# Kernel tuning notes

Hardware: AMD Instinct MI355X
Metric: run time of the kernel (lower is better)

Reference implementation:

```python
import jax, jax.numpy as jnp
import numpy as np
from jax.ops import segment_sum, segment_max

N_NODES = 10000
N_EDGES = 160000
N_GRAPHS = 32
IN_DIM = 128
HID = 256
HEADS = 4


def setup_inputs() -> dict:
    key = jax.random.key(0)
    ks = jax.random.split(key, 12)
    x = jax.random.normal(ks[0], (N_NODES, IN_DIM), dtype=jnp.float32)
    edge_index = jax.random.randint(ks[1], (2, N_EDGES), 0, N_NODES, dtype=jnp.int64)
    batch = jnp.sort(jax.random.randint(ks[2], (N_NODES,), 0, N_GRAPHS, dtype=jnp.int64))
    s = 0.05
    params = {
        "W1": jax.random.normal(ks[3], (IN_DIM, HID), dtype=jnp.float32) * s,
        "b1": jnp.zeros((HID,), dtype=jnp.float32),
        "W2": jax.random.normal(ks[4], (HID, HID), dtype=jnp.float32) * s,
        "b2": jnp.zeros((HID,), dtype=jnp.float32),
        "Wg": jax.random.normal(ks[5], (HID, HEADS * HID), dtype=jnp.float32) * s,
        "att_src": jax.random.normal(ks[6], (HEADS, HID), dtype=jnp.float32) * s,
        "att_dst": jax.random.normal(ks[7], (HEADS, HID), dtype=jnp.float32) * s,
        "bg": jnp.zeros((HID,), dtype=jnp.float32),
        "W_heads": jax.random.normal(ks[8], (HID, 4), dtype=jnp.float32) * s,
        "b_heads": jnp.zeros((4,), dtype=jnp.float32),
    }
    return {"x": x, "edge_index": edge_index, "batch": batch, **params}


def _add_self_loops(edge_index, n):
    loop = jnp.arange(n, dtype=edge_index.dtype)
    src = jnp.concatenate([edge_index[0], loop])
    dst = jnp.concatenate([edge_index[1], loop])
    return src, dst


def _gcn_conv(x, W, b, src, dst, n):
    # PyG GCNConv: add self-loops, symmetric normalization D^-1/2 A D^-1/2
    h = x @ W                                   # [N, out]
    deg = segment_sum(jnp.ones_like(src, dtype=h.dtype), dst, num_segments=n)
    dinv = jax.lax.rsqrt(jnp.maximum(deg, 1e-12))
    coef = dinv[src] * dinv[dst]                # [E+N]
    out = segment_sum(h[src] * coef[:, None], dst, num_segments=n)
    return out + b


def _gat_conv(x, Wg, att_src, att_dst, bg, src, dst, n):
    # PyG GATConv(heads=4, concat=False): mean over heads, leaky_relu slope 0.2
    h = (x @ Wg).reshape(n, HEADS, HID)         # [N, H, C]
    a_src = jnp.einsum('nhc,hc->nh', h, att_src)
    a_dst = jnp.einsum('nhc,hc->nh', h, att_dst)
    e = jax.nn.leaky_relu(a_src[src] + a_dst[dst], 0.2)   # [E+N, H]
    m = segment_max(e, dst, num_segments=n)
    e = jnp.exp(e - m[dst])
    z = segment_sum(e, dst, num_segments=n)
    alpha = e / (z[dst] + 1e-16)                # softmax over edges into each dst
    out = segment_sum(h[src] * alpha[:, :, None], dst, num_segments=n)  # [N, H, C]
    return out.mean(axis=1) + bg


def reference(x, edge_index, batch, W1, b1, W2, b2, Wg, att_src, att_dst, bg, W_heads, b_heads):
    n = x.shape[0]
    src, dst = _add_self_loops(edge_index, n)
    h1 = jax.nn.relu(_gcn_conv(x, W1, b1, src, dst, n))
    h2 = jax.nn.relu(_gcn_conv(h1, W2, b2, src, dst, n))
    h3 = jax.nn.relu(_gat_conv(h2, Wg, att_src, att_dst, bg, src, dst, n))
    # global_mean_pool
    ones = jnp.ones((n,), dtype=h3.dtype)
    cnt = segment_sum(ones, batch, num_segments=N_GRAPHS)
    pooled = segment_sum(h3, batch, num_segments=N_GRAPHS) / jnp.maximum(cnt, 1.0)[:, None]
    # four scalar heads stacked: cols = [energy_absorption, elastic_modulus, ballistic_limit, penetration_resistance]
    return pooled @ W_heads + b_heads           # [G, 4]
```

## Files before the change

kernel.cpp:

```cpp
#include <hip/hip_runtime.h>
#include <cmath>

#define IN_DIM 128
#define HID 256
#define NHEADS 4
#define NGRAPHS 32

typedef unsigned short u16;
typedef __attribute__((ext_vector_type(8))) short bfrag8;
typedef __attribute__((ext_vector_type(4))) float f32x4;

__device__ __forceinline__ u16 f2bf(float x) {
  unsigned u = __float_as_uint(x);
  unsigned r = (u + 0x7fffu + ((u >> 16) & 1u)) >> 16;
  return (u16)r;
}
__device__ __forceinline__ float bf2f(u16 v) {
  return __uint_as_float(((unsigned)v) << 16);
}
__device__ __forceinline__ float lof(unsigned u) { return __uint_as_float(u << 16); }
__device__ __forceinline__ float hif(unsigned u) { return __uint_as_float(u & 0xffff0000u); }
__device__ __forceinline__ float lrelu02(float x) { return x > 0.f ? x : 0.2f * x; }

#define GACC(U, W)                                                   \
  acc[0] += (W) * lof((U).x); acc[1] += (W) * hif((U).x);            \
  acc[2] += (W) * lof((U).y); acc[3] += (W) * hif((U).y);            \
  acc[4] += (W) * lof((U).z); acc[5] += (W) * hif((U).z);            \
  acc[6] += (W) * lof((U).w); acc[7] += (W) * hif((U).w);

__global__ __launch_bounds__(256) void count_edges_k(const int* __restrict__ dst,
                                                     int* __restrict__ cnt, int E) {
  int i = blockIdx.x * 256 + threadIdx.x;
  if (i < E) atomicAdd(&cnt[dst[i]], 1);
}

__global__ __launch_bounds__(1024) void scan_k(const int* __restrict__ cnt,
                                               int* __restrict__ row_ptr,
                                               float* __restrict__ dinv, int n) {
  __shared__ int s_w[16];
  __shared__ int s_tot;
  int tid = threadIdx.x;
  int wv = tid >> 6, lane = tid & 63;
  int carry = 0;
  int nch = (n + 1023) >> 10;
  for (int c = 0; c < nch; c++) {
    int i = (c << 10) + tid;
    int v = (i < n) ? cnt[i] : 0;
    int incl = v;
    #pragma unroll
    for (int off = 1; off < 64; off <<= 1) {
      int t = __shfl_up(incl, off);
      if (lane >= off) incl += t;
    }
    if (lane == 63) s_w[wv] = incl;
    __syncthreads();
    if (tid < 16) {
      int sv = s_w[tid];
      int si = sv;
      #pragma unroll
      for (int off = 1; off < 16; off <<= 1) {
        int t = __shfl_up(si, off, 16);
        if (tid >= off) si += t;
      }
      s_w[tid] = si - sv;
      if (tid == 15) s_tot = si;
    }
    __syncthreads();
    int excl = incl - v + s_w[wv] + carry;
    if (i < n) {
      row_ptr[i] = excl;
      dinv[i] = rsqrtf((float)(v + 1));
    }
    carry += s_tot;
    __syncthreads();
  }
  if (tid == 0) row_ptr[n] = carry;
}

__global__ __launch_bounds__(256) void fill_csr_k(const int* __restrict__ src,
                                                  const int* __restrict__ dst,
                                                  const int* __restrict__ row_ptr,
                                                  int* __restrict__ cursor,
                                                  int* __restrict__ csr_src, int E) {
  int i = blockIdx.x * 256 + threadIdx.x;
  if (i < E) {
    int d = dst[i];
    int p = atomicAdd(&cursor[d], 1);
    csr_src[row_ptr[d] + p] = src[i];
  }
}

__device__ void pack_a_dev(const float* __restrict__ A, u16* __restrict__ Ap,
                           int K, int KT, int wid, int lane) {
  int fm = wid / KT, kt = wid - fm * KT;
  int m = fm * 16 + (lane & 15);
  int kb = kt * 32 + (lane >> 4) * 8;
  const float* src = A + (size_t)m * K + kb;
  float4 v0 = *(const float4*)src;
  float4 v1 = *(const float4*)(src + 4);
  float vv[8] = {v0.x, v0.y, v0.z, v0.w, v1.x, v1.y, v1.z, v1.w};
  u16 hi[8], lo[8];
  #pragma unroll
  for (int j = 0; j < 8; j++) {
    u16 h = f2bf(vv[j]);
    hi[j] = h;
    lo[j] = f2bf(vv[j] - bf2f(h));
  }
  u16* dstp = Ap + ((size_t)fm * KT + kt) * 1024 + lane * 8;
  *(ushort4*)(dstp)       = make_ushort4(hi[0], hi[1], hi[2], hi[3]);
  *(ushort4*)(dstp + 4)   = make_ushort4(hi[4], hi[5], hi[6], hi[7]);
  *(ushort4*)(dstp + 512) = make_ushort4(lo[0], lo[1], lo[2], lo[3]);
  *(ushort4*)(dstp + 516) = make_ushort4(lo[4], lo[5], lo[6], lo[7]);
}

__device__ void pack_b_dev(const float* __restrict__ B, u16* __restrict__ Bp,
                           int N, int KT, int wid, int lane) {
  int fn = wid / KT, kt = wid - fn * KT;
  int n = fn * 16 + (lane & 15);
  int kb = kt * 32 + (lane >> 4) * 8;
  float vv[8];
  #pragma unroll
  for (int j = 0; j < 8; j++) vv[j] = B[(size_t)(kb + j) * N + n];
  u16 hi[8], lo[8];
  #pragma unroll
  for (int j = 0; j < 8; j++) {
    u16 h = f2bf(vv[j]);
    hi[j] = h;
    lo[j] = f2bf(vv[j] - bf2f(h));
  }
  u16* dstp = Bp + ((size_t)fn * KT + kt) * 1024 + lane * 8;
  *(ushort4*)(dstp)       = make_ushort4(hi[0], hi[1], hi[2], hi[3]);
  *(ushort4*)(dstp + 4)   = make_ushort4(hi[4], hi[5], hi[6], hi[7]);
  *(ushort4*)(dstp + 512) = make_ushort4(lo[0], lo[1], lo[2], lo[3]);
  *(ushort4*)(dstp + 516) = make_ushort4(lo[4], lo[5], lo[6], lo[7]);
}

__global__ __launch_bounds__(256) void prep_k(const float* __restrict__ x,
                                              const float* __restrict__ W1,
                                              const float* __restrict__ W2,
                                              const float* __restrict__ Wg,
                                              const float* __restrict__ att_src,
                                              const float* __restrict__ att_dst,
                                              u16* __restrict__ xp,
                                              u16* __restrict__ w1p,
                                              u16* __restrict__ w2p,
                                              u16* __restrict__ wgp,
                                              float* __restrict__ w_s,
                                              float* __restrict__ w_d, int NFM) {
  __shared__ float red_s[4][NHEADS];
  __shared__ float red_d[4][NHEADS];
  int b = blockIdx.x;
  int tid = threadIdx.x;
  int lane = tid & 63;
  int XB = NFM;
  if (b < XB) {
    int wid = b * 4 + (tid >> 6);
    if (wid < NFM * 4) pack_a_dev(x, xp, IN_DIM, 4, wid, lane);
  } else if (b < XB + 16) {
    pack_b_dev(W1, w1p, HID, 4, (b - XB) * 4 + (tid >> 6), lane);
  } else if (b < XB + 48) {
    pack_b_dev(W2, w2p, HID, 8, (b - XB - 16) * 4 + (tid >> 6), lane);
  } else if (b < XB + 176) {
    pack_b_dev(Wg, wgp, NHEADS * HID, 8, (b - XB - 48) * 4 + (tid >> 6), lane);
  } else {
    int k = b - (XB + 176);
    int c = tid, wvv = c >> 6, ln = c & 63;
    #pragma unroll
    for (int h = 0; h < NHEADS; h++) {
      float w = Wg[(size_t)k * (NHEADS * HID) + h * HID + c];
      float vs = w * att_src[h * HID + c];
      float vd = w * att_dst[h * HID + c];
      #pragma unroll
      for (int off = 32; off; off >>= 1) {
        vs += __shfl_xor(vs, off);
        vd += __shfl_xor(vd, off);
      }
      if (ln == 0) { red_s[wvv][h] = vs; red_d[wvv][h] = vd; }
    }
    __syncthreads();
    if (c < NHEADS)
      w_s[k * NHEADS + c] = red_s[0][c] + red_s[1][c] + red_s[2][c] + red_s[3][c];
    else if (c < 2 * NHEADS) {
      int h = c - NHEADS;
      w_d[k * NHEADS + h] = red_d[0][h] + red_d[1][h] + red_d[2][h] + red_d[3][h];
    }
  }
}

template <int KT, int LDC, bool ALO>
__global__ __launch_bounds__(256) void mfma_gemm_k(const u16* __restrict__ Ap,
                                                   const u16* __restrict__ Bp,
                                                   u16* __restrict__ Cb, int M) {
  int tid = threadIdx.x;
  int w = tid >> 6, lane = tid & 63;
  int wm = w >> 1, wn = w & 1;
  int fm0 = blockIdx.y * 4 + wm * 2;
  int fn0 = blockIdx.x * 4 + wn * 2;
  f32x4 acc[2][2] = {};
  #pragma unroll
  for (int kt = 0; kt < KT; kt++) {
    bfrag8 a_hi[2], a_lo[2], b_hi[2], b_lo[2];
    #pragma unroll
    for (int f = 0; f < 2; f++) {
      const u16* pa = Ap + ((size_t)(fm0 + f) * KT + kt) * 1024 + lane * 8;
      a_hi[f] = *(const bfrag8*)pa;
      if constexpr (ALO) a_lo[f] = *(const bfrag8*)(pa + 512);
      const u16* pb = Bp + ((size_t)(fn0 + f) * KT + kt) * 1024 + lane * 8;
      b_hi[f] = *(const bfrag8*)pb;
      b_lo[f] = *(const bfrag8*)(pb + 512);
    }
    #pragma unroll
    for (int f = 0; f < 2; f++) {
      #pragma unroll
      for (int g = 0; g < 2; g++) {
        acc[f][g] = __builtin_amdgcn_mfma_f32_16x16x32_bf16(a_hi[f], b_hi[g], acc[f][g], 0, 0, 0);
        acc[f][g] = __builtin_amdgcn_mfma_f32_16x16x32_bf16(a_hi[f], b_lo[g], acc[f][g], 0, 0, 0);
        if constexpr (ALO)
          acc[f][g] = __builtin_amdgcn_mfma_f32_16x16x32_bf16(a_lo[f], b_hi[g], acc[f][g], 0, 0, 0);
      }
    }
  }
  int r0 = (lane >> 4) * 4;
  int cl = lane & 15;
  #pragma unroll
  for (int f = 0; f < 2; f++) {
    #pragma unroll
    for (int g = 0; g < 2; g++) {
      int col = (fn0 + g) * 16 + cl;
      #pragma unroll
      for (int r = 0; r < 4; r++) {
        int row = (fm0 + f) * 16 + r0 + r;
        if (row < M) Cb[(size_t)row * LDC + col] = f2bf(acc[f][g][r]);
      }
    }
  }
}

template <bool LOGITS, bool PACK_LO>
__global__ __launch_bounds__(256) void gcn_agg_k(const u16* __restrict__ t,
                                                 const int* __restrict__ row_ptr,
                                                 const int* __restrict__ csr_src,
                                                 const float* __restrict__ dinv,
                                                 const float* __restrict__ bias,
                                                 u16* __restrict__ apack,
                                                 const float* __restrict__ w_s,
                                                 const float* __restrict__ w_d,
                                                 float4* __restrict__ a_src4,
                                                 float4* __restrict__ a_dst4, int N) {
  int wv = threadIdx.x >> 6, lane = threadIdx.x & 63;
  int i = blockIdx.x * 4 + wv;
  if (i >= N) return;
  float di = dinv[i];
  int half = lane >> 5;
  int c8 = (lane & 31) * 8;
  int beg = row_ptr[i], end = row_ptr[i + 1];
  float acc[8];
  if (half == 0) {
    uint4 u = *(const uint4*)&t[(size_t)i * HID + c8];
    float w = di * di;
    acc[0] = w * lof(u.x); acc[1] = w * hif(u.x);
    acc[2] = w * lof(u.y); acc[3] = w * hif(u.y);
    acc[4] = w * lof(u.z); acc[5] = w * hif(u.z);
    acc[6] = w * lof(u.w); acc[7] = w * hif(u.w);
  } else {
    #pragma unroll
    for (int j = 0; j < 8; j++) acc[j] = 0.f;
  }
  int e = beg + half;
  for (; e + 2 < end; e += 4) {
    int s0 = csr_src[e], s1 = csr_src[e + 2];
    float w0 = dinv[s0] * di, w1 = dinv[s1] * di;
    uint4 u0 = *(const uint4*)&t[(size_t)s0 * HID + c8];
    uint4 u1 = *(const uint4*)&t[(size_t)s1 * HID + c8];
    GACC(u0, w0);
    GACC(u1, w1);
  }
  if (e < end) {
    int s = csr_src[e];
    float w = dinv[s] * di;
    uint4 u = *(const uint4*)&t[(size_t)s * HID + c8];
    GACC(u, w);
  }
  #pragma unroll
  for (int j = 0; j < 8; j++) acc[j] += __shfl_xor(acc[j], 32);
  float4 b0 = *(const float4*)&bias[c8];
  float4 b1 = *(const float4*)&bias[c8 + 4];
  float v[8];
  v[0] = fmaxf(acc[0] + b0.x, 0.f); v[1] = fmaxf(acc[1] + b0.y, 0.f);
  v[2] = fmaxf(acc[2] + b0.z, 0.f); v[3] = fmaxf(acc[3] + b0.w, 0.f);
  v[4] = fmaxf(acc[4] + b1.x, 0.f); v[5] = fmaxf(acc[5] + b1.y, 0.f);
  v[6] = fmaxf(acc[6] + b1.z, 0.f); v[7] = fmaxf(acc[7] + b1.w, 0.f);
  if (half == 0) {
    int fm = i >> 4, kt = c8 >> 5;
    int pl = (i & 15) + 16 * ((c8 >> 3) & 3);
    size_t base = ((size_t)fm * 8 + kt) * 1024 + pl * 8;
    u16 h[8];
    #pragma unroll
    for (int j = 0; j < 8; j++) h[j] = f2bf(v[j]);
    *(ushort4*)&apack[base]     = make_ushort4(h[0], h[1], h[2], h[3]);
    *(ushort4*)&apack[base + 4] = make_ushort4(h[4], h[5], h[6], h[7]);
    if constexpr (PACK_LO) {
      *(ushort4*)&apack[base + 512] =
          make_ushort4(f2bf(v[0] - bf2f(h[0])), f2bf(v[1] - bf2f(h[1])),
                       f2bf(v[2] - bf2f(h[2])), f2bf(v[3] - bf2f(h[3])));
      *(ushort4*)&apack[base + 516] =
          make_ushort4(f2bf(v[4] - bf2f(h[4])), f2bf(v[5] - bf2f(h[5])),
                       f2bf(v[6] - bf2f(h[6])), f2bf(v[7] - bf2f(h[7])));
    }
  }
  if constexpr (LOGITS) {
    float ps0 = 0.f, ps1 = 0.f, ps2 = 0.f, ps3 = 0.f;
    float pd0 = 0.f, pd1 = 0.f, pd2 = 0.f, pd3 = 0.f;
    #pragma unroll
    for (int j = 0; j < 8; j++) {
      float4 sv = *(const float4*)&w_s[(c8 + j) * NHEADS];
      float4 dv = *(const float4*)&w_d[(c8 + j) * NHEADS];
      float vj = v[j];
      ps0 += vj * sv.x; ps1 += vj * sv.y; ps2 += vj * sv.z; ps3 += vj * sv.w;
      pd0 += vj * dv.x; pd1 += vj * dv.y; pd2 += vj * dv.z; pd3 += vj * dv.w;
    }
    #pragma unroll
    for (int off = 16; off; off >>= 1) {
      ps0 += __shfl_xor(ps0, off); ps1 += __shfl_xor(ps1, off);
      ps2 += __shfl_xor(ps2, off); ps3 += __shfl_xor(ps3, off);
      pd0 += __shfl_xor(pd0, off); pd1 += __shfl_xor(pd1, off);
      pd2 += __shfl_xor(pd2, off); pd3 += __shfl_xor(pd3, off);
    }
    if (lane == 0) {
      a_src4[i] = make_float4(ps0, ps1, ps2, ps3);
      a_dst4[i] = make_float4(pd0, pd1, pd2, pd3);
    }
  }
}

__global__ __launch_bounds__(256) void gat_agg_k(const u16* __restrict__ hgT,
                                                 const int* __restrict__ row_ptr,
                                                 const int* __restrict__ csr_src,
                                                 const float4* __restrict__ a_src4,
                                                 const float4* __restrict__ a_dst4,
                                                 const float* __restrict__ bg,
                                                 float* __restrict__ out, int N) {
  __shared__ int s_src[4][64];
  __shared__ float s_al[4][2][64];
  __shared__ float s_comb[2][32][9];
  int wv = threadIdx.x >> 6, lane = threadIdx.x & 63;
  int nodeSlot = wv >> 1, half = wv & 1;
  int i = blockIdx.x * 2 + nodeSlot;
  if (i >= N) { __syncthreads(); return; }
  int beg = row_ptr[i], end = row_ptr[i + 1];
  int deg = end - beg;
  float4 ad = a_dst4[i];
  int hsel = lane >> 5;
  const u16* rowbase = hgT + half * 512 + lane * 8;
  float acc[8];
  #pragma unroll
  for (int j = 0; j < 8; j++) acc[j] = 0.f;

  if (deg <= 63) {
    int s = (lane < deg) ? csr_src[beg + lane] : i;
    bool valid = (lane <= deg);
    float4 as = a_src4[s];
    float l0 = valid ? lrelu02(as.x + ad.x) : -INFINITY;
    float l1 = valid ? lrelu02(as.y + ad.y) : -INFINITY;
    float l2 = valid ? lrelu02(as.z + ad.z) : -INFINITY;
    float l3 = valid ? lrelu02(as.w + ad.w) : -INFINITY;
    float m0 = l0, m1 = l1, m2 = l2, m3 = l3;
    #pragma unroll
    for (int off = 32; off; off >>= 1) {
      m0 = fmaxf(m0, __shfl_xor(m0, off)); m1 = fmaxf(m1, __shfl_xor(m1, off));
      m2 = fmaxf(m2, __shfl_xor(m2, off)); m3 = fmaxf(m3, __shfl_xor(m3, off));
    }
    float e0 = valid ? expf(l0 - m0) : 0.f;
    float e1 = valid ? expf(l1 - m1) : 0.f;
    float e2 = valid ? expf(l2 - m2) : 0.f;
    float e3 = valid ? expf(l3 - m3) : 0.f;
    float z0 = e0, z1 = e1, z2 = e2, z3 = e3;
    #pragma unroll
    for (int off = 32; off; off >>= 1) {
      z0 += __shfl_xor(z0, off); z1 += __shfl_xor(z1, off);
      z2 += __shfl_xor(z2, off); z3 += __shfl_xor(z3, off);
    }
    s_src[wv][lane] = s;
    if (half == 0) {
      s_al[wv][0][lane] = e0 / (z0 + 1e-16f);
      s_al[wv][1][lane] = e1 / (z1 + 1e-16f);
    } else {
      s_al[wv][0][lane] = e2 / (z2 + 1e-16f);
      s_al[wv][1][lane] = e3 / (z3 + 1e-16f);
    }
    int nk = deg + 1;
    int e = 0;
    for (; e + 3 < nk; e += 4) {
      int sa = s_src[wv][e + 0], sb = s_src[wv][e + 1];
      int sc = s_src[wv][e + 2], sd = s_src[wv][e + 3];
      float wa = s_al[wv][hsel][e + 0], wb = s_al[wv][hsel][e + 1];
      float wc = s_al[wv][hsel][e + 2], wd = s_al[wv][hsel][e + 3];
      uint4 ua = *(const uint4*)(rowbase + (size_t)sa * 1024);
      uint4 ub = *(const uint4*)(rowbase + (size_t)sb * 1024);
      uint4 uc = *(const uint4*)(rowbase + (size_t)sc * 1024);
      uint4 ud = *(const uint4*)(rowbase + (size_t)sd * 1024);
      GACC(ua, wa); GACC(ub, wb); GACC(uc, wc); GACC(ud, wd);
    }
    for (; e < nk; e++) {
      int sa = s_src[wv][e];
      float wa = s_al[wv][hsel][e];
      uint4 ua = *(const uint4*)(rowbase + (size_t)sa * 1024);
      GACC(ua, wa);
    }
  } else {
    float4 asi = a_src4[i];
    float ls0 = lrelu02(asi.x + ad.x), ls1 = lrelu02(asi.y + ad.y);
    float ls2 = lrelu02(asi.z + ad.z), ls3 = lrelu02(asi.w + ad.w);
    float m0 = ls0, m1 = ls1, m2 = ls2, m3 = ls3;
    for (int e = beg + lane; e < end; e += 64) {
      float4 as = a_src4[csr_src[e]];
      m0 = fmaxf(m0, lrelu02(as.x + ad.x)); m1 = fmaxf(m1, lrelu02(as.y + ad.y));
      m2 = fmaxf(m2, lrelu02(as.z + ad.z)); m3 = fmaxf(m3, lrelu02(as.w + ad.w));
    }
    #pragma unroll
    for (int off = 32; off; off >>= 1) {
      m0 = fmaxf(m0, __shfl_xor(m0, off)); m1 = fmaxf(m1, __shfl_xor(m1, off));
      m2 = fmaxf(m2, __shfl_xor(m2, off)); m3 = fmaxf(m3, __shfl_xor(m3, off));
    }
    float z0 = (lane == 0) ? expf(ls0 - m0) : 0.f;
    float z1 = (lane == 0) ? expf(ls1 - m1) : 0.f;
    float z2 = (lane == 0) ? expf(ls2 - m2) : 0.f;
    float z3 = (lane == 0) ? expf(ls3 - m3) : 0.f;
    for (int e = beg + lane; e < end; e += 64) {
      float4 as = a_src4[csr_src[e]];
      z0 += expf(lrelu02(as.x + ad.x) - m0); z1 += expf(lrelu02(as.y + ad.y) - m1);
      z2 += expf(lrelu02(as.z + ad.z) - m2); z3 += expf(lrelu02(as.w + ad.w) - m3);
    }
    #pragma unroll
    for (int off = 32; off; off >>= 1) {
      z0 += __shfl_xor(z0, off); z1 += __shfl_xor(z1, off);
      z2 += __shfl_xor(z2, off); z3 += __shfl_xor(z3, off);
    }
    float iz0 = 1.f / (z0 + 1e-16f), iz1 = 1.f / (z1 + 1e-16f);
    float iz2 = 1.f / (z2 + 1e-16f), iz3 = 1.f / (z3 + 1e-16f);
    {
      float w0 = expf(ls0 - m0) * iz0, w1 = expf(ls1 - m1) * iz1;
      float w2 = expf(ls2 - m2) * iz2, w3 = expf(ls3 - m3) * iz3;
      float aw = (half == 0) ? (hsel == 0 ? w0 : w1) : (hsel == 0 ? w2 : w3);
      uint4 u = *(const uint4*)(rowbase + (size_t)i * 1024);
      GACC(u, aw);
    }
    for (int base = beg; base < end; base += 64) {
      int mc = min(64, end - base);
      if (lane < mc) {
        int s = csr_src[base + lane];
        float4 as = a_src4[s];
        s_src[wv][lane] = s;
        if (half == 0) {
          s_al[wv][0][lane] = expf(lrelu02(as.x + ad.x) - m0) * iz0;
          s_al[wv][1][lane] = expf(lrelu02(as.y + ad.y) - m1) * iz1;
        } else {
          s_al[wv][0][lane] = expf(lrelu02(as.z + ad.z) - m2) * iz2;
          s_al[wv][1][lane] = expf(lrelu02(as.w + ad.w) - m3) * iz3;
        }
      }
      for (int e = 0; e < mc; e++) {
        int sa = s_src[wv][e];
        float wa = s_al[wv][hsel][e];
        uint4 ua = *(const uint4*)(rowbase + (size_t)sa * 1024);
        GACC(ua, wa);
      }
    }
  }
  #pragma unroll
  for (int j = 0; j < 8; j++) acc[j] += __shfl_xor(acc[j], 32);
  if (half == 1 && lane < 32) {
    #pragma unroll
    for (int j = 0; j < 8; j++) s_comb[nodeSlot][lane][j] = acc[j];
  }
  __syncthreads();
  if (half == 0 && lane < 32) {
    int cb = lane * 8;
    float o[8];
    #pragma unroll
    for (int j = 0; j < 8; j++)
      o[j] = fmaxf((acc[j] + s_comb[nodeSlot][lane][j]) * 0.25f + bg[cb + j], 0.f);
    float* op = out + (size_t)i * HID + cb;
    *(float4*)(op + 0) = make_float4(o[0], o[1], o[2], o[3]);
    *(float4*)(op + 4) = make_float4(o[4], o[5], o[6], o[7]);
  }
}

#define POOL_CHUNK 50
__global__ __launch_bounds__(256) void pool_acc_k(const float* __restrict__ h3,
                                                  const int* __restrict__ batch,
                                                  float* __restrict__ pooled,
                                                  float* __restrict__ gcnt, int N) {
  int c = threadIdx.x;
  int i0 = blockIdx.x * POOL_CHUNK;
  int i1 = min(i0 + POOL_CHUNK, N);
  if (i0 >= N) return;
  float acc = 0.f;
  int cur = batch[i0];
  int cnt_local = 0;
  for (int i = i0; i < i1; i++) {
    int g = batch[i];
    if (g != cur) {
      atomicAdd(&pooled[cur * HID + c], acc);
      if (c == 0) atomicAdd(&gcnt[cur], (float)cnt_local);
      acc = 0.f;
      cnt_local = 0;
      cur = g;
    }
    acc += h3[(size_t)i * HID + c];
    cnt_local++;
  }
  atomicAdd(&pooled[cur * HID + c], acc);
  if (c == 0) atomicAdd(&gcnt[cur], (float)cnt_local);
}

__global__ __launch_bounds__(128) void head_k(const float* __restrict__ pooled,
                                              const float* __restrict__ gcnt,
                                              const float* __restrict__ W_heads,
                                              const float* __restrict__ b_heads,
                                              float* __restrict__ out) {
  int tid = threadIdx.x;
  if (tid >= NGRAPHS * 4) return;
  int g = tid >> 2, k = tid & 3;
  float invc = 1.f / fmaxf(gcnt[g], 1.f);
  float acc = 0.f;
  for (int c = 0; c < HID; c++) acc += pooled[g * HID + c] * W_heads[c * 4 + k];
  out[g * 4 + k] = acc * invc + b_heads[k];
}

extern "C" void kernel_launch(void* const* d_in, const int* in_sizes, int n_in,
                              void* d_out, int out_size, void* d_ws, size_t ws_size,
                              hipStream_t stream) {
  const float* x = (const float*)d_in[0];
  const int* ei = (const int*)d_in[1];
  const int* batch = (const int*)d_in[2];
  const float* W1 = (const float*)d_in[3];
  const float* b1 = (const float*)d_in[4];
  const float* W2 = (const float*)d_in[5];
  const float* b2 = (const float*)d_in[6];
  const float* Wg = (const float*)d_in[7];
  const float* att_src = (const float*)d_in[8];
  const float* att_dst = (const float*)d_in[9];
  const float* bg = (const float*)d_in[10];
  const float* W_heads = (const float*)d_in[11];
  const float* b_heads = (const float*)d_in[12];
  float* out = (float*)d_out;

  const int N = in_sizes[0] / IN_DIM;
  const int E = in_sizes[1] / 2;
  const int* src = ei;
  const int* dst = ei + E;

  const int NFM = N / 16;
  const int NFMP = ((N + 63) / 64) * 4;

  char* ws = (char*)d_ws;
  size_t off = 0;
  auto take = [&](size_t bytes) -> char* {
    char* p = ws + off;
    off = (off + bytes + 255) & ~(size_t)255;
    return p;
  };
  int* cnt      = (int*)take((size_t)N * 4);
  int* cursor   = (int*)take((size_t)N * 4);
  float* pooled = (float*)take((size_t)NGRAPHS * HID * 4 + NGRAPHS * 4);
  float* gcnt   = pooled + NGRAPHS * HID;
  size_t zero_span = off;
  int* row_ptr  = (int*)take((size_t)(N + 1) * 4);
  int* csr_src  = (int*)take((size_t)E * 4);
  float* dinv   = (float*)take((size_t)N * 4);
  float4* a_src4 = (float4*)take((size_t)N * 16);
  float4* a_dst4 = (float4*)take((size_t)N * 16);
  float* w_s    = (float*)take((size_t)HID * NHEADS * 4);
  float* w_d    = (float*)take((size_t)HID * NHEADS * 4);
  u16*   tb     = (u16*)take((size_t)N * HID * 2);
  float* h3     = (float*)take((size_t)N * HID * 4);
  u16*   hgT    = (u16*)take((size_t)N * NHEADS * HID * 2);
  u16*   xp     = (u16*)take((size_t)NFMP * 4 * 1024 * 2);
  u16*   h1p    = (u16*)take((size_t)NFMP * 8 * 1024 * 2);
  u16*   h2p    = (u16*)take((size_t)NFMP * 8 * 1024 * 2);
  u16*   w1p    = (u16*)take((size_t)16 * 4 * 1024 * 2);
  u16*   w2p    = (u16*)take((size_t)16 * 8 * 1024 * 2);
  u16*   wgp    = (u16*)take((size_t)64 * 8 * 1024 * 2);

  hipMemsetAsync(cnt, 0, zero_span, stream);

  int eb = (E + 255) / 256;
  count_edges_k<<<eb, 256, 0, stream>>>(dst, cnt, E);
  scan_k<<<1, 1024, 0, stream>>>(cnt, row_ptr, dinv, N);
  fill_csr_k<<<eb, 256, 0, stream>>>(src, dst, row_ptr, cursor, csr_src, E);
  prep_k<<<NFM + 176 + 256, 256, 0, stream>>>(x, W1, W2, Wg, att_src, att_dst,
                                              xp, w1p, w2p, wgp, w_s, w_d, NFM);

  int mg64 = (N + 63) / 64;
  int ng4 = (N + 3) / 4;
  int ng2 = (N + 1) / 2;
  mfma_gemm_k<4, HID, true><<<dim3(4, mg64), 256, 0, stream>>>(xp, w1p, tb, N);
  gcn_agg_k<false, true><<<ng4, 256, 0, stream>>>(tb, row_ptr, csr_src, dinv, b1,
                                                  h1p, nullptr, nullptr, nullptr, nullptr, N);
  mfma_gemm_k<8, HID, true><<<dim3(4, mg64), 256, 0, stream>>>(h1p, w2p, tb, N);
  gcn_agg_k<true, false><<<ng4, 256, 0, stream>>>(tb, row_ptr, csr_src, dinv, b2,
                                                  h2p, w_s, w_d, a_src4, a_dst4, N);
  mfma_gemm_k<8, NHEADS * HID, false><<<dim3(16, mg64), 256, 0, stream>>>(h2p, wgp, hgT, N);
  gat_agg_k<<<ng2, 256, 0, stream>>>(hgT, row_ptr, csr_src, a_src4, a_dst4, bg, h3, N);
  int pb = (N + POOL_CHUNK - 1) / POOL_CHUNK;
  pool_acc_k<<<pb, 256, 0, stream>>>(h3, batch, pooled, gcnt, N);
  head_k<<<1, 128, 0, stream>>>(pooled, gcnt, W_heads, b_heads, out);
}
```

Measured before the change: 209.0 us.

## Fold CSR scan into prep kernel and restructure GCN aggregation with wave-wide edge lists

Removes the separate single-block scan launch by running the prefix scan as block 0 of the prep kernel. The scan now uses 256 threads instead of 1024, so it takes more loop iterations. The GCN aggregation now has each full wave own a node with 4 columns per lane. For nodes with degree up to 64, the wave loads neighbor indices and weights once into lanes and broadcasts them by shuffle. The first GCN pass also bitonic-sorts each node's neighbor list and writes it back, so later passes gather in a more cache-friendly order. This adds sort and shuffle overhead, and it changes the fp32 summation order, so results can differ slightly in rounding.

```diff
diff --git a/kernel.cpp b/kernel.cpp
--- a/kernel.cpp
+++ b/kernel.cpp
@@ -28,53 +28,14 @@
   acc[4] += (W) * lof((U).z); acc[5] += (W) * hif((U).z);            \
   acc[6] += (W) * lof((U).w); acc[7] += (W) * hif((U).w);
 
+#define GACC2(U, W)                                                  \
+  a0 += (W) * lof((U).x); a1 += (W) * hif((U).x);                    \
+  a2 += (W) * lof((U).y); a3 += (W) * hif((U).y);
+
 __global__ __launch_bounds__(256) void count_edges_k(const int* __restrict__ dst,
                                                      int* __restrict__ cnt, int E) {
   int i = blockIdx.x * 256 + threadIdx.x;
   if (i < E) atomicAdd(&cnt[dst[i]], 1);
-}
-
-__global__ __launch_bounds__(1024) void scan_k(const int* __restrict__ cnt,
-                                               int* __restrict__ row_ptr,
-                                               float* __restrict__ dinv, int n) {
-  __shared__ int s_w[16];
-  __shared__ int s_tot;
-  int tid = threadIdx.x;
-  int wv = tid >> 6, lane = tid & 63;
-  int carry = 0;
-  int nch = (n + 1023) >> 10;
-  for (int c = 0; c < nch; c++) {
-    int i = (c << 10) + tid;
-    int v = (i < n) ? cnt[i] : 0;
-    int incl = v;
-    #pragma unroll
-    for (int off = 1; off < 64; off <<= 1) {
-      int t = __shfl_up(incl, off);
-      if (lane >= off) incl += t;
-    }
-    if (lane == 63) s_w[wv] = incl;
-    __syncthreads();
-    if (tid < 16) {
-      int sv = s_w[tid];
-      int si = sv;
-      #pragma unroll
-      for (int off = 1; off < 16; off <<= 1) {
-        int t = __shfl_up(si, off, 16);
-        if (tid >= off) si += t;
-      }
-      s_w[tid] = si - sv;
-      if (tid == 15) s_tot = si;
-    }
-    __syncthreads();
-    int excl = incl - v + s_w[wv] + carry;
-    if (i < n) {
-      row_ptr[i] = excl;
-      dinv[i] = rsqrtf((float)(v + 1));
-    }
-    carry += s_tot;
-    __syncthreads();
-  }
-  if (tid == 0) row_ptr[n] = carry;
 }
 
 __global__ __launch_bounds__(256) void fill_csr_k(const int* __restrict__ src,
@@ -88,6 +49,42 @@
     int p = atomicAdd(&cursor[d], 1);
     csr_src[row_ptr[d] + p] = src[i];
   }
+}
+
+__device__ void scan_dev(const int* __restrict__ cnt, int* __restrict__ row_ptr,
+                         float* __restrict__ dinv, int n) {
+  __shared__ int s_w[4];
+  __shared__ int s_off[4];
+  __shared__ int s_tot;
+  int tid = threadIdx.x, wv = tid >> 6, lane = tid & 63;
+  int carry = 0;
+  int nch = (n + 255) >> 8;
+  for (int c = 0; c < nch; c++) {
+    int i = (c << 8) + tid;
+    int v = (i < n) ? cnt[i] : 0;
+    int incl = v;
+    #pragma unroll
+    for (int off = 1; off < 64; off <<= 1) {
+      int t = __shfl_up(incl, off);
+      if (lane >= off) incl += t;
+    }
+    if (lane == 63) s_w[wv] = incl;
+    __syncthreads();
+    if (tid == 0) {
+      int a0 = s_w[0], a1 = s_w[1], a2 = s_w[2], a3 = s_w[3];
+      s_off[0] = 0; s_off[1] = a0; s_off[2] = a0 + a1; s_off[3] = a0 + a1 + a2;
+      s_tot = a0 + a1 + a2 + a3;
+    }
+    __syncthreads();
+    int excl = incl - v + s_off[wv] + carry;
+    if (i < n) {
+      row_ptr[i] = excl;
+      dinv[i] = rsqrtf((float)(v + 1));
+    }
+    carry += s_tot;
+    __syncthreads();
+  }
+  if (tid == 0) row_ptr[n] = carry;
 }
 
 __device__ void pack_a_dev(const float* __restrict__ A, u16* __restrict__ Ap,
@@ -141,17 +138,26 @@
                                               const float* __restrict__ Wg,
                                               const float* __restrict__ att_src,
                                               const float* __restrict__ att_dst,
+                                              const int* __restrict__ cnt,
+                                              int* __restrict__ row_ptr,
+                                              float* __restrict__ dinv,
                                               u16* __restrict__ xp,
                                               u16* __restrict__ w1p,
                                               u16* __restrict__ w2p,
                                               u16* __restrict__ wgp,
                                               float* __restrict__ w_s,
-                                              float* __restrict__ w_d, int NFM) {
+                                              float* __restrict__ w_d,
+                                              int NFM, int N) {
   __shared__ float red_s[4][NHEADS];
   __shared__ float red_d[4][NHEADS];
   int b = blockIdx.x;
   int tid = threadIdx.x;
   int lane = tid & 63;
+  if (b == 0) {
+    scan_dev(cnt, row_ptr, dinv, N);
+    return;
+  }
+  b -= 1;
   int XB = NFM;
   if (b < XB) {
     int wid = b * 4 + (tid >> 6);
@@ -236,10 +242,10 @@
   }
 }
 
-template <bool LOGITS, bool PACK_LO>
+template <bool LOGITS, bool PACK_LO, bool SORT>
 __global__ __launch_bounds__(256) void gcn_agg_k(const u16* __restrict__ t,
                                                  const int* __restrict__ row_ptr,
-                                                 const int* __restrict__ csr_src,
+                                                 int* __restrict__ csr_src,
                                                  const float* __restrict__ dinv,
                                                  const float* __restrict__ bias,
                                                  u16* __restrict__ apack,
@@ -251,76 +257,102 @@
   int i = blockIdx.x * 4 + wv;
   if (i >= N) return;
   float di = dinv[i];
-  int half = lane >> 5;
-  int c8 = (lane & 31) * 8;
+  int c4 = lane * 4;
   int beg = row_ptr[i], end = row_ptr[i + 1];
-  float acc[8];
-  if (half == 0) {
-    uint4 u = *(const uint4*)&t[(size_t)i * HID + c8];
+  int deg = end - beg;
+  float a0, a1, a2, a3;
+  {
+    uint2 u = *(const uint2*)&t[(size_t)i * HID + c4];
     float w = di * di;
-    acc[0] = w * lof(u.x); acc[1] = w * hif(u.x);
-    acc[2] = w * lof(u.y); acc[3] = w * hif(u.y);
-    acc[4] = w * lof(u.z); acc[5] = w * hif(u.z);
-    acc[6] = w * lof(u.w); acc[7] = w * hif(u.w);
+    a0 = w * lof(u.x); a1 = w * hif(u.x); a2 = w * lof(u.y); a3 = w * hif(u.y);
+  }
+  if (deg <= 64) {
+    int s = (lane < deg) ? csr_src[beg + lane] : 0x7fffffff;
+    if constexpr (SORT) {
+      if (deg > 1) {
+        #pragma unroll
+        for (int k = 2; k <= 64; k <<= 1) {
+          #pragma unroll
+          for (int j = k >> 1; j > 0; j >>= 1) {
+            int vp = __shfl_xor(s, j);
+            bool lower = ((lane & j) == 0);
+            bool up = ((lane & k) == 0);
+            int mn = min(s, vp), mx = max(s, vp);
+            s = (lower == up) ? mn : mx;
+          }
+        }
+        if (lane < deg) csr_src[beg + lane] = s;
+      }
+    }
+    float w = (lane < deg) ? dinv[s] * di : 0.f;
+    int e = 0;
+    for (; e + 3 < deg; e += 4) {
+      int s0 = __shfl(s, e), s1 = __shfl(s, e + 1);
+      int s2 = __shfl(s, e + 2), s3 = __shfl(s, e + 3);
+      float w0 = __shfl(w, e), w1 = __shfl(w, e + 1);
+      float w2 = __shfl(w, e + 2), w3 = __shfl(w, e + 3);
+      uint2 u0 = *(const uint2*)&t[(size_t)s0 * HID + c4];
+      uint2 u1 = *(const uint2*)&t[(size_t)s1 * HID + c4];
+      uint2 u2 = *(const uint2*)&t[(size_t)s2 * HID + c4];
+      uint2 u3 = *(const uint2*)&t[(size_t)s3 * HID + c4];
+      GACC2(u0, w0); GACC2(u1, w1); GACC2(u2, w2); GACC2(u3, w3);
+    }
+    for (; e < deg; e++) {
+      int s0 = __shfl(s, e);
+      float w0 = __shfl(w, e);
+      uint2 u = *(const uint2*)&t[(size_t)s0 * HID + c4];
+      GACC2(u, w0);
+    }
   } else {
-    #pragma unroll
-    for (int j = 0; j < 8; j++) acc[j] = 0.f;
-  }
-  int e = beg + half;
-  for (; e + 2 < end; e += 4) {
-    int s0 = csr_src[e], s1 = csr_src[e + 2];
-    float w0 = dinv[s0] * di, w1 = dinv[s1] * di;
-    uint4 u0 = *(const uint4*)&t[(size_t)s0 * HID + c8];
-    uint4 u1 = *(const uint4*)&t[(size_t)s1 * HID + c8];
-    GACC(u0, w0);
-    GACC(u1, w1);
-  }
-  if (e < end) {
-    int s = csr_src[e];
-    float w = dinv[s] * di;
-    uint4 u = *(const uint4*)&t[(size_t)s * HID + c8];
-    GACC(u, w);
-  }
-  #pragma unroll
-  for (int j = 0; j < 8; j++) acc[j] += __shfl_xor(acc[j], 32);
-  float4 b0 = *(const float4*)&bias[c8];
-  float4 b1 = *(const float4*)&bias[c8 + 4];
-  float v[8];
-  v[0] = fmaxf(acc[0] + b0.x, 0.f); v[1] = fmaxf(acc[1] + b0.y, 0.f);
-  v[2] = fmaxf(acc[2] + b0.z, 0.f); v[3] = fmaxf(acc[3] + b0.w, 0.f);
-  v[4] = fmaxf(acc[4] + b1.x, 0.f); v[5] = fmaxf(acc[5] + b1.y, 0.f);
-  v[6] = fmaxf(acc[6] + b1.z, 0.f); v[7] = fmaxf(acc[7] + b1.w, 0.f);
-  if (half == 0) {
-    int fm = i >> 4, kt = c8 >> 5;
-    int pl = (i & 15) + 16 * ((c8 >> 3) & 3);
-    size_t base = ((size_t)fm * 8 + kt) * 1024 + pl * 8;
-    u16 h[8];
-    #pragma unroll
-    for (int j = 0; j < 8; j++) h[j] = f2bf(v[j]);
-    *(ushort4*)&apack[base]     = make_ushort4(h[0], h[1], h[2], h[3]);
-    *(ushort4*)&apack[base + 4] = make_ushort4(h[4], h[5], h[6], h[7]);
-    if constexpr (PACK_LO) {
+    int e = beg;
+    for (; e + 3 < end; e += 4) {
+      int s0 = csr_src[e + 0], s1 = csr_src[e + 1];
+      int s2 = csr_src[e + 2], s3 = csr_src[e + 3];
+      float w0 = dinv[s0] * di, w1 = dinv[s1] * di;
+      float w2 = dinv[s2] * di, w3 = dinv[s3] * di;
+      uint2 u0 = *(const uint2*)&t[(size_t)s0 * HID + c4];
+      uint2 u1 = *(const uint2*)&t[(size_t)s1 * HID + c4];
+      uint2 u2 = *(const uint2*)&t[(size_t)s2 * HID + c4];
+      uint2 u3 = *(const uint2*)&t[(size_t)s3 * HID + c4];
+      GACC2(u0, w0); GACC2(u1, w1); GACC2(u2, w2); GACC2(u3, w3);
+    }
+    for (; e < end; e++) {
+      int s = csr_src[e];
+      float w = dinv[s] * di;
+      uint2 u = *(const uint2*)&t[(size_t)s * HID + c4];
+      GACC2(u, w);
+    }
+  }
+  float4 bv = *(const float4*)&bias[c4];
+  float v0 = fmaxf(a0 + bv.x, 0.f), v1 = fmaxf(a1 + bv.y, 0.f);
+  float v2 = fmaxf(a2 + bv.z, 0.f), v3 = fmaxf(a3 + bv.w, 0.f);
+  {
+    int fm = i >> 4, kt = c4 >> 5;
+    int pl = (i & 15) + 16 * ((c4 >> 3) & 3);
+    int j = c4 & 7;
+    size_t base = ((size_t)fm * 8 + kt) * 1024 + pl * 8 + j;
+    u16 h0 = f2bf(v0), h1 = f2bf(v1), h2 = f2bf(v2), h3 = f2bf(v3);
+    *(ushort4*)&apack[base] = make_ushort4(h0, h1, h2, h3);
+    if constexpr (PACK_LO)
       *(ushort4*)&apack[base + 512] =
-          make_ushort4(f2bf(v[0] - bf2f(h[0])), f2bf(v[1] - bf2f(h[1])),
-                       f2bf(v[2] - bf2f(h[2])), f2bf(v[3] - bf2f(h[3])));
-      *(ushort4*)&apack[base + 516] =
-          make_ushort4(f2bf(v[4] - bf2f(h[4])), f2bf(v[5] - bf2f(h[5])),
-                       f2bf(v[6] - bf2f(h[6])), f2bf(v[7] - bf2f(h[7])));
-    }
+          make_ushort4(f2bf(v0 - bf2f(h0)), f2bf(v1 - bf2f(h1)),
+                       f2bf(v2 - bf2f(h2)), f2bf(v3 - bf2f(h3)));
   }
   if constexpr (LOGITS) {
-    float ps0 = 0.f, ps1 = 0.f, ps2 = 0.f, ps3 = 0.f;
-    float pd0 = 0.f, pd1 = 0.f, pd2 = 0.f, pd3 = 0.f;
-    #pragma unroll
-    for (int j = 0; j < 8; j++) {
-      float4 sv = *(const float4*)&w_s[(c8 + j) * NHEADS];
-      float4 dv = *(const float4*)&w_d[(c8 + j) * NHEADS];
-      float vj = v[j];
-      ps0 += vj * sv.x; ps1 += vj * sv.y; ps2 += vj * sv.z; ps3 += vj * sv.w;
-      pd0 += vj * dv.x; pd1 += vj * dv.y; pd2 += vj * dv.z; pd3 += vj * dv.w;
-    }
-    #pragma unroll
-    for (int off = 16; off; off >>= 1) {
+    const float4* ws4 = (const float4*)w_s;
+    const float4* wd4 = (const float4*)w_d;
+    float4 s0 = ws4[c4 + 0], s1 = ws4[c4 + 1], s2 = ws4[c4 + 2], s3 = ws4[c4 + 3];
+    float4 d0 = wd4[c4 + 0], d1 = wd4[c4 + 1], d2 = wd4[c4 + 2], d3 = wd4[c4 + 3];
+    float ps0 = v0 * s0.x + v1 * s1.x + v2 * s2.x + v3 * s3.x;
+    float ps1 = v0 * s0.y + v1 * s1.y + v2 * s2.y + v3 * s3.y;
+    float ps2 = v0 * s0.z + v1 * s1.z + v2 * s2.z + v3 * s3.z;
+    float ps3 = v0 * s0.w + v1 * s1.w + v2 * s2.w + v3 * s3.w;
+    float pd0 = v0 * d0.x + v1 * d1.x + v2 * d2.x + v3 * d3.x;
+    float pd1 = v0 * d0.y + v1 * d1.y + v2 * d2.y + v3 * d3.y;
+    float pd2 = v0 * d0.z + v1 * d1.z + v2 * d2.z + v3 * d3.z;
+    float pd3 = v0 * d0.w + v1 * d1.w + v2 * d2.w + v3 * d3.w;
+    #pragma unroll
+    for (int off = 32; off; off >>= 1) {
       ps0 += __shfl_xor(ps0, off); ps1 += __shfl_xor(ps1, off);
       ps2 += __shfl_xor(ps2, off); ps3 += __shfl_xor(ps3, off);
       pd0 += __shfl_xor(pd0, off); pd1 += __shfl_xor(pd1, off);
@@ -587,20 +619,20 @@
 
   int eb = (E + 255) / 256;
   count_edges_k<<<eb, 256, 0, stream>>>(dst, cnt, E);
-  scan_k<<<1, 1024, 0, stream>>>(cnt, row_ptr, dinv, N);
+  prep_k<<<1 + NFM + 176 + 256, 256, 0, stream>>>(x, W1, W2, Wg, att_src, att_dst,
+                                                  cnt, row_ptr, dinv,
+                                                  xp, w1p, w2p, wgp, w_s, w_d, NFM, N);
   fill_csr_k<<<eb, 256, 0, stream>>>(src, dst, row_ptr, cursor, csr_src, E);
-  prep_k<<<NFM + 176 + 256, 256, 0, stream>>>(x, W1, W2, Wg, att_src, att_dst,
-                                              xp, w1p, w2p, wgp, w_s, w_d, NFM);
 
   int mg64 = (N + 63) / 64;
   int ng4 = (N + 3) / 4;
   int ng2 = (N + 1) / 2;
   mfma_gemm_k<4, HID, true><<<dim3(4, mg64), 256, 0, stream>>>(xp, w1p, tb, N);
-  gcn_agg_k<false, true><<<ng4, 256, 0, stream>>>(tb, row_ptr, csr_src, dinv, b1,
-                                                  h1p, nullptr, nullptr, nullptr, nullptr, N);
+  gcn_agg_k<false, true, true><<<ng4, 256, 0, stream>>>(tb, row_ptr, csr_src, dinv, b1,
+                                                        h1p, nullptr, nullptr, nullptr, nullptr, N);
   mfma_gemm_k<8, HID, true><<<dim3(4, mg64), 256, 0, stream>>>(h1p, w2p, tb, N);
-  gcn_agg_k<true, false><<<ng4, 256, 0, stream>>>(tb, row_ptr, csr_src, dinv, b2,
-                                                  h2p, w_s, w_d, a_src4, a_dst4, N);
+  gcn_agg_k<true, false, false><<<ng4, 256, 0, stream>>>(tb, row_ptr, csr_src, dinv, b2,
+                                                         h2p, w_s, w_d, a_src4, a_dst4, N);
   mfma_gemm_k<8, NHEADS * HID, false><<<dim3(16, mg64), 256, 0, stream>>>(h2p, wgp, hgT, N);
   gat_agg_k<<<ng2, 256, 0, stream>>>(hgT, row_ptr, csr_src, a_src4, a_dst4, bg, h3, N);
   int pb = (N + POOL_CHUNK - 1) / POOL_CHUNK;
```

Result: no change. 205.2 us (-1.8%).
